# Kernel optimization log

Hardware: AMD Instinct MI355X
Metric: run time of the kernel (lower is better)

Reference implementation:

```python
import jax, jax.numpy as jnp
import numpy as np

MAX_WORDS = 256  # = batch['labels'].shape[1]


def _align(hidden, word_ids, max_words):
    """Batched segment-mean: (B,S,D) subtoken states -> (B,max_words,D) word states.
    Equivalent to align_subtokens_to_words applied per sample (word_ids all valid)."""
    B, S, D = hidden.shape
    seg = (word_ids.astype(jnp.int32) + jnp.arange(B, dtype=jnp.int32)[:, None] * max_words).reshape(-1)
    sums = jax.ops.segment_sum(hidden.reshape(-1, D), seg, num_segments=B * max_words)
    cnts = jax.ops.segment_sum(jnp.ones((B * S,), hidden.dtype), seg, num_segments=B * max_words)
    out = jnp.where(cnts[:, None] > 0, sums / jnp.maximum(cnts, 1.0)[:, None], 0.0)
    return out.reshape(B, max_words, D)


def setup_inputs() -> dict:
    key = jax.random.key(0)
    ks = jax.random.split(key, 8)
    B, S, D, W = 64, 512, 768, MAX_WORDS
    h_hing_sub = jax.random.normal(ks[0], (B, S, D), dtype=jnp.float32)
    h_rob_sub = jax.random.normal(ks[1], (B, S, D), dtype=jnp.float32)
    hing_word_ids = jnp.sort(jax.random.randint(ks[2], (B, S), 0, W), axis=-1).astype(jnp.int32)
    rob_word_ids = jnp.sort(jax.random.randint(ks[3], (B, S), 0, W), axis=-1).astype(jnp.int32)
    num_words = jax.random.randint(ks[4], (B,), 1, W).astype(jnp.int32)
    router_w1 = jax.random.normal(ks[5], (2 * D, 256), dtype=jnp.float32) * (1.0 / np.sqrt(2 * D))
    router_b1 = jnp.zeros((256,), jnp.float32)
    router_w2 = jax.random.normal(ks[6], (256, 1), dtype=jnp.float32) * (1.0 / 16.0)
    router_b2 = jnp.zeros((1,), jnp.float32)
    head_w = jax.random.normal(ks[7], (D, 7), dtype=jnp.float32) * (1.0 / np.sqrt(D))
    head_b = jnp.zeros((7,), jnp.float32)
    return {
        'h_hing_sub': h_hing_sub, 'h_rob_sub': h_rob_sub,
        'hing_word_ids': hing_word_ids, 'rob_word_ids': rob_word_ids,
        'num_words': num_words,
        'router_w1': router_w1, 'router_b1': router_b1,
        'router_w2': router_w2, 'router_b2': router_b2,
        'head_w': head_w, 'head_b': head_b,
    }


def reference(h_hing_sub, h_rob_sub, hing_word_ids, rob_word_ids, num_words,
              router_w1, router_b1, router_w2, router_b2, head_w, head_b):
    W = MAX_WORDS
    # scatter-mean subtokens -> words (the dominant custom-kernel op)
    h_hing = _align(h_hing_sub, hing_word_ids, W)   # (B, W, 768)
    h_rob = _align(h_rob_sub, rob_word_ids, W)      # (B, W, 768)
    # token-level MLP router on concatenated word states (router_input='both')
    router_in = jnp.concatenate([h_hing, h_rob], axis=-1)             # (B, W, 1536)
    hdn = jax.nn.relu(jnp.einsum('bwd,dh->bwh', router_in, router_w1) + router_b1)
    alpha = jax.nn.sigmoid(jnp.einsum('bwh,ho->bwo', hdn, router_w2) + router_b2)  # (B, W, 1)
    blended = alpha * h_hing + (1.0 - alpha) * h_rob                  # (B, W, 768)
    logits = jnp.einsum('bwd,dl->bwl', blended, head_w) + head_b      # (B, W, num_labels)
    l2_disagreement = jnp.linalg.norm(h_hing - h_rob, axis=-1)        # (B, W)
    return logits, alpha.squeeze(-1), l2_disagreement
```

## Files before the change

kernel.cpp:

```cpp
#include <hip/hip_runtime.h>
#include <hip/hip_bf16.h>
#include <math.h>

#define BATCH 64
#define SEQ   512
#define DIM   768
#define NW    256
#define NT    (BATCH * NW)
#define KDIM  1536
#define HID   256
#define NL    7

#define BM  32
#define BK  64
#define BKP 72
#define NKT (KDIM / BK)

typedef __bf16 bf16_t;
typedef bf16_t bf16x4 __attribute__((ext_vector_type(4)));
typedef bf16_t bf16x8 __attribute__((ext_vector_type(8)));
typedef float  f32x4  __attribute__((ext_vector_type(4)));

__device__ __forceinline__ void madv(f32x4& a, const f32x4& v, float s) {
    a[0] = fmaf(v[0], s, a[0]);
    a[1] = fmaf(v[1], s, a[1]);
    a[2] = fmaf(v[2], s, a[2]);
    a[3] = fmaf(v[3], s, a[3]);
}

__global__ __launch_bounds__(256) void convert_w1_kernel(
    const float* __restrict__ w1, bf16_t* __restrict__ w1t)
{
    int kc = blockIdx.x >> 3;
    int kg = blockIdx.x & 7;
    int n  = threadIdx.x;
    bf16x8 v;
    #pragma unroll
    for (int j = 0; j < 8; j++)
        v[j] = (bf16_t)w1[(size_t)(kc * 64 + kg * 8 + j) * HID + n];
    *(bf16x8*)(w1t + (size_t)kc * (HID * BK) + n * BK + kg * 8) = v;
}

__global__ __launch_bounds__(256) void starts_kernel(
    const int* __restrict__ idh, const int* __restrict__ idr,
    int* __restrict__ starts)
{
    int blk = blockIdx.x;
    int t = blk >> 6;
    int b = blk & 63;
    const int* ids = (t ? idr : idh) + b * SEQ;
    int w = threadIdx.x;
    int lo = 0, hi = SEQ;
    while (lo < hi) {
        int m = (lo + hi) >> 1;
        if (ids[m] < w) lo = m + 1; else hi = m;
    }
    int* row = starts + blk * 257;
    row[w] = lo;
    if (w == 0) row[256] = SEQ;
}

__global__ __launch_bounds__(256, 2) void align_kernel(
    const float* __restrict__ hh, const float* __restrict__ hr,
    const int* __restrict__ starts, bf16_t* __restrict__ X)
{
    int tid  = threadIdx.x;
    int lane = tid & 63;
    int wv   = tid >> 6;
    int task = blockIdx.x * 4 + wv;
    int b = task >> 7;
    int t = (task >> 6) & 1;
    int c = task & 63;
    int w0 = c * 4;

    const int*   st    = starts + (t * 64 + b) * 257;
    const f32x4* base4 = (const f32x4*)((t ? hr : hh) + (size_t)b * SEQ * DIM);
    bf16_t*      dstb  = X + (size_t)b * NW * KDIM + t * DIM;

    int lo = st[w0];
    #pragma unroll 1
    for (int w = w0; w < w0 + 4; w++) {
        int hi = st[w + 1];
        int ns = __builtin_amdgcn_readfirstlane(hi - lo);
        bf16_t* xr = dstb + (size_t)w * KDIM;

        if (ns <= 0) {
            bf16x4 z = {};
            *(bf16x4*)(xr + lane * 4)         = z;
            *(bf16x4*)(xr + (lane + 64) * 4)  = z;
            *(bf16x4*)(xr + (lane + 128) * 4) = z;
        } else {
            int nm1 = ns - 1;
            const f32x4* p0 = base4 + (size_t)lo * 192;
            const f32x4* p1 = base4 + (size_t)(lo + (1 < ns ? 1 : nm1)) * 192;
            const f32x4* p2 = base4 + (size_t)(lo + (2 < ns ? 2 : nm1)) * 192;
            const f32x4* p3 = base4 + (size_t)(lo + (3 < ns ? 3 : nm1)) * 192;
            const f32x4* p4 = base4 + (size_t)(lo + (4 < ns ? 4 : nm1)) * 192;
            const f32x4* p5 = base4 + (size_t)(lo + (5 < ns ? 5 : nm1)) * 192;

            f32x4 l0a = p0[lane], l0b = p0[lane + 64], l0c = p0[lane + 128];
            f32x4 l1a = p1[lane], l1b = p1[lane + 64], l1c = p1[lane + 128];
            f32x4 l2a = p2[lane], l2b = p2[lane + 64], l2c = p2[lane + 128];
            f32x4 l3a = p3[lane], l3b = p3[lane + 64], l3c = p3[lane + 128];
            f32x4 l4a = p4[lane], l4b = p4[lane + 64], l4c = p4[lane + 128];
            f32x4 l5a = p5[lane], l5b = p5[lane + 64], l5c = p5[lane + 128];

            float k1 = (1 < ns) ? 1.f : 0.f;
            float k2 = (2 < ns) ? 1.f : 0.f;
            float k3 = (3 < ns) ? 1.f : 0.f;
            float k4 = (4 < ns) ? 1.f : 0.f;
            float k5 = (5 < ns) ? 1.f : 0.f;

            f32x4 a0 = l0a, a1 = l0b, a2 = l0c;
            madv(a0, l1a, k1); madv(a1, l1b, k1); madv(a2, l1c, k1);
            madv(a0, l2a, k2); madv(a1, l2b, k2); madv(a2, l2c, k2);
            madv(a0, l3a, k3); madv(a1, l3b, k3); madv(a2, l3c, k3);
            madv(a0, l4a, k4); madv(a1, l4b, k4); madv(a2, l4c, k4);
            madv(a0, l5a, k5); madv(a1, l5b, k5); madv(a2, l5c, k5);

            if (ns > 6) {
                for (int s = lo + 6; s < lo + ns; s++) {
                    const f32x4* r = base4 + (size_t)s * 192;
                    a0 += r[lane]; a1 += r[lane + 64]; a2 += r[lane + 128];
                }
            }

            float inv = 1.0f / (float)ns;
            bf16x4 o0, o1, o2;
            #pragma unroll
            for (int e = 0; e < 4; e++) {
                o0[e] = (bf16_t)(a0[e] * inv);
                o1[e] = (bf16_t)(a1[e] * inv);
                o2[e] = (bf16_t)(a2[e] * inv);
            }
            *(bf16x4*)(xr + lane * 4)         = o0;
            *(bf16x4*)(xr + (lane + 64) * 4)  = o1;
            *(bf16x4*)(xr + (lane + 128) * 4) = o2;
        }
        lo = hi;
    }
}

__global__ __launch_bounds__(256) void gemm_alpha_kernel(
    const bf16_t* __restrict__ X, const bf16_t* __restrict__ w1t,
    const float* __restrict__ b1, const float* __restrict__ w2,
    const float* __restrict__ b2, float* __restrict__ out)
{
    __shared__ __align__(16) bf16_t Xs[BM][BKP];
    __shared__ __align__(16) bf16_t Ws[HID][BKP];
    __shared__ float alpha_acc[BM];

    int tid   = threadIdx.x;
    int lane  = tid & 63;
    int wv    = tid >> 6;
    int row16 = lane & 15;
    int quad  = lane >> 4;
    int tok0  = blockIdx.x * BM;

    f32x4 acc[2][4];
    #pragma unroll
    for (int mi = 0; mi < 2; mi++)
        #pragma unroll
        for (int ni = 0; ni < 4; ni++)
            acc[mi][ni] = (f32x4){0.f, 0.f, 0.f, 0.f};

    int xr = tid >> 3;
    int xc = tid & 7;

    for (int kc = 0; kc < NKT; kc++) {
        {
            const uint4* src = (const uint4*)(X + (size_t)(tok0 + xr) * KDIM + kc * BK + xc * 8);
            *(uint4*)(&Xs[xr][xc * 8]) = *src;
        }
        {
            const uint4* srcb = (const uint4*)(w1t + (size_t)kc * (HID * BK));
            #pragma unroll
            for (int i = 0; i < 8; i++) {
                int cidx = tid + i * 256;
                *(uint4*)(&Ws[cidx >> 3][(cidx & 7) * 8]) = srcb[cidx];
            }
        }
        __syncthreads();
        #pragma unroll
        for (int kk2 = 0; kk2 < 2; kk2++) {
            bf16x8 af[2], bfg[4];
            #pragma unroll
            for (int mi = 0; mi < 2; mi++)
                af[mi] = *(const bf16x8*)(&Xs[mi * 16 + row16][kk2 * 32 + quad * 8]);
            #pragma unroll
            for (int ni = 0; ni < 4; ni++)
                bfg[ni] = *(const bf16x8*)(&Ws[wv * 64 + ni * 16 + row16][kk2 * 32 + quad * 8]);
            #pragma unroll
            for (int mi = 0; mi < 2; mi++)
                #pragma unroll
                for (int ni = 0; ni < 4; ni++)
                    acc[mi][ni] = __builtin_amdgcn_mfma_f32_16x16x32_bf16(
                        af[mi], bfg[ni], acc[mi][ni], 0, 0, 0);
        }
        __syncthreads();
    }

    float w2v[4], b1v[4];
    #pragma unroll
    for (int ni = 0; ni < 4; ni++) {
        int col = wv * 64 + ni * 16 + row16;
        w2v[ni] = w2[col];
        b1v[ni] = b1[col];
    }
    if (tid < BM) alpha_acc[tid] = 0.f;
    __syncthreads();

    #pragma unroll
    for (int mi = 0; mi < 2; mi++) {
        #pragma unroll
        for (int r = 0; r < 4; r++) {
            float p = 0.f;
            #pragma unroll
            for (int ni = 0; ni < 4; ni++) {
                float v = acc[mi][ni][r] + b1v[ni];
                v = v > 0.f ? v : 0.f;
                p += v * w2v[ni];
            }
            p += __shfl_xor(p, 1);
            p += __shfl_xor(p, 2);
            p += __shfl_xor(p, 4);
            p += __shfl_xor(p, 8);
            if (row16 == 0)
                atomicAdd(&alpha_acc[mi * 16 + quad * 4 + r], p);
        }
    }
    __syncthreads();
    if (tid < BM) {
        float a = 1.f / (1.f + expf(-(alpha_acc[tid] + b2[0])));
        out[(size_t)NT * NL + tok0 + tid] = a;
    }
}

__global__ __launch_bounds__(256) void blend_kernel(
    const bf16_t* __restrict__ X, const float* __restrict__ hw,
    const float* __restrict__ hb, float* __restrict__ out)
{
    __shared__ float hws[NL * DIM];
    int tid  = threadIdx.x;
    int lane = tid & 63;
    int wv   = tid >> 6;

    for (int i = tid; i < DIM * NL; i += 256) {
        int d = i / NL, l = i - d * NL;
        hws[l * DIM + d] = hw[i];
    }
    __syncthreads();

    int g   = lane >> 3;
    int u   = lane & 7;
    int tok = blockIdx.x * 32 + wv * 8 + g;

    float a = out[(size_t)NT * NL + tok];
    const bf16_t* xrow = X + (size_t)tok * KDIM;

    float lg[NL] = {0.f, 0.f, 0.f, 0.f, 0.f, 0.f, 0.f};
    float l2 = 0.f;

    #pragma unroll
    for (int k = 0; k < 12; k++) {
        int d0 = (k * 8 + u) * 8;
        bf16x8 hp = *(const bf16x8*)(xrow + d0);
        bf16x8 rp = *(const bf16x8*)(xrow + DIM + d0);
        float bl[8];
        #pragma unroll
        for (int e = 0; e < 8; e++) {
            float hhv = (float)hp[e];
            float hrv = (float)rp[e];
            float df  = hhv - hrv;
            bl[e] = fmaf(a, df, hrv);
            l2 = fmaf(df, df, l2);
        }
        #pragma unroll
        for (int l = 0; l < NL; l++) {
            f32x4 wA = *(const f32x4*)(&hws[l * DIM + d0]);
            f32x4 wB = *(const f32x4*)(&hws[l * DIM + d0 + 4]);
            lg[l] += bl[0]*wA[0] + bl[1]*wA[1] + bl[2]*wA[2] + bl[3]*wA[3]
                   + bl[4]*wB[0] + bl[5]*wB[1] + bl[6]*wB[2] + bl[7]*wB[3];
        }
    }

    #pragma unroll
    for (int off = 1; off < 8; off <<= 1) {
        #pragma unroll
        for (int l = 0; l < NL; l++) lg[l] += __shfl_xor(lg[l], off);
        l2 += __shfl_xor(l2, off);
    }

    if (u < NL) {
        float v = (u == 0) ? lg[0] : (u == 1) ? lg[1] : (u == 2) ? lg[2]
                : (u == 3) ? lg[3] : (u == 4) ? lg[4] : (u == 5) ? lg[5] : lg[6];
        out[(size_t)tok * NL + u] = v + hb[u];
    } else {
        out[(size_t)NT * NL + NT + tok] = sqrtf(l2);
    }
}

extern "C" void kernel_launch(void* const* d_in, const int* in_sizes, int n_in,
                              void* d_out, int out_size, void* d_ws, size_t ws_size,
                              hipStream_t stream)
{
    const float* hh  = (const float*)d_in[0];
    const float* hr  = (const float*)d_in[1];
    const int*   idh = (const int*)d_in[2];
    const int*   idr = (const int*)d_in[3];
    const float* w1  = (const float*)d_in[5];
    const float* b1  = (const float*)d_in[6];
    const float* w2  = (const float*)d_in[7];
    const float* b2  = (const float*)d_in[8];
    const float* hw  = (const float*)d_in[9];
    const float* hb  = (const float*)d_in[10];
    float* out = (float*)d_out;

    bf16_t* X      = (bf16_t*)d_ws;
    bf16_t* w1t    = X + (size_t)NT * KDIM;
    int*    starts = (int*)(w1t + (size_t)NKT * HID * BK);

    convert_w1_kernel<<<192, 256, 0, stream>>>(w1, w1t);
    starts_kernel<<<128, 256, 0, stream>>>(idh, idr, starts);
    align_kernel<<<2048, 256, 0, stream>>>(hh, hr, starts, X);
    gemm_alpha_kernel<<<NT / BM, 256, 0, stream>>>(X, w1t, b1, w2, b2, out);
    blend_kernel<<<512, 256, 0, stream>>>(X, hw, hb, out);
}
```

Baseline: 291.1 us.

## Fuse router GEMM with blend/head and restructure align as streaming segment scan

Folds the blend/logits/L2 stage into the router GEMM kernel, which now uses 512 threads and 64-token tiles. The blend step reads alpha from shared memory and reuses the W1 tile buffer to hold the head weights, so one launch and the alpha round-trip through global memory go away. The align kernel now has each wave stream a contiguous subtoken range covering 32 words over a 256-element slice of the hidden dimension. It reads word ids through readlane, flushes a mean whenever the word changes, and zero-fills empty words. This cuts per-word launch overhead and keeps loads sequential, at the cost of serialized boundary handling and fewer blocks.

```diff
diff --git a/kernel.cpp b/kernel.cpp
--- a/kernel.cpp
+++ b/kernel.cpp
@@ -11,7 +11,7 @@
 #define HID   256
 #define NL    7
 
-#define BM  32
+#define BM  64
 #define BK  64
 #define BKP 72
 #define NKT (KDIM / BK)
@@ -20,13 +20,6 @@
 typedef bf16_t bf16x4 __attribute__((ext_vector_type(4)));
 typedef bf16_t bf16x8 __attribute__((ext_vector_type(8)));
 typedef float  f32x4  __attribute__((ext_vector_type(4)));
-
-__device__ __forceinline__ void madv(f32x4& a, const f32x4& v, float s) {
-    a[0] = fmaf(v[0], s, a[0]);
-    a[1] = fmaf(v[1], s, a[1]);
-    a[2] = fmaf(v[2], s, a[2]);
-    a[3] = fmaf(v[3], s, a[3]);
-}
 
 __global__ __launch_bounds__(256) void convert_w1_kernel(
     const float* __restrict__ w1, bf16_t* __restrict__ w1t)
@@ -60,99 +53,100 @@
     if (w == 0) row[256] = SEQ;
 }
 
-__global__ __launch_bounds__(256, 2) void align_kernel(
+__global__ __launch_bounds__(256) void align_kernel(
     const float* __restrict__ hh, const float* __restrict__ hr,
+    const int* __restrict__ idh, const int* __restrict__ idr,
     const int* __restrict__ starts, bf16_t* __restrict__ X)
 {
     int tid  = threadIdx.x;
     int lane = tid & 63;
     int wv   = tid >> 6;
     int task = blockIdx.x * 4 + wv;
-    int b = task >> 7;
-    int t = (task >> 6) & 1;
-    int c = task & 63;
-    int w0 = c * 4;
-
-    const int*   st    = starts + (t * 64 + b) * 257;
-    const f32x4* base4 = (const f32x4*)((t ? hr : hh) + (size_t)b * SEQ * DIM);
-    bf16_t*      dstb  = X + (size_t)b * NW * KDIM + t * DIM;
-
-    int lo = st[w0];
-    #pragma unroll 1
-    for (int w = w0; w < w0 + 4; w++) {
-        int hi = st[w + 1];
-        int ns = __builtin_amdgcn_readfirstlane(hi - lo);
-        bf16_t* xr = dstb + (size_t)w * KDIM;
-
-        if (ns <= 0) {
+    int q  = task & 7;
+    int r3 = task >> 3;
+    int sl = r3 % 3;
+    int bt = r3 / 3;
+    int b  = bt >> 1;
+    int t  = bt & 1;
+    int w0 = q * 32;
+
+    const int*   st   = starts + (t * 64 + b) * 257;
+    const int*   ids  = (t ? idr : idh) + b * SEQ;
+    const f32x4* base = (const f32x4*)((t ? hr : hh) + (size_t)b * SEQ * DIM) + sl * 64;
+    bf16_t*      dst  = X + (size_t)b * NW * KDIM + t * DIM + sl * 256 + lane * 4;
+
+    int sLo = st[w0];
+    int sHi = st[w0 + 32];
+
+    f32x4 acc = {0.f, 0.f, 0.f, 0.f};
+    int   cnt = 0;
+    int   w   = w0;
+
+    for (int sb = sLo; sb < sHi; sb += 8) {
+        int smax = sHi - 1;
+        f32x4 v0 = base[(size_t)(sb     < smax ? sb     : smax) * 192 + lane];
+        f32x4 v1 = base[(size_t)(sb + 1 < smax ? sb + 1 : smax) * 192 + lane];
+        f32x4 v2 = base[(size_t)(sb + 2 < smax ? sb + 2 : smax) * 192 + lane];
+        f32x4 v3 = base[(size_t)(sb + 3 < smax ? sb + 3 : smax) * 192 + lane];
+        f32x4 v4 = base[(size_t)(sb + 4 < smax ? sb + 4 : smax) * 192 + lane];
+        f32x4 v5 = base[(size_t)(sb + 5 < smax ? sb + 5 : smax) * 192 + lane];
+        f32x4 v6 = base[(size_t)(sb + 6 < smax ? sb + 6 : smax) * 192 + lane];
+        f32x4 v7 = base[(size_t)(sb + 7 < smax ? sb + 7 : smax) * 192 + lane];
+        int myid = ids[(lane & 7) + sb < sHi ? (lane & 7) + sb : smax];
+
+        f32x4 vv[8] = {v0, v1, v2, v3, v4, v5, v6, v7};
+        #pragma unroll
+        for (int j = 0; j < 8; j++) {
+            int s = sb + j;
+            if (s >= sHi) break;
+            int wid = __builtin_amdgcn_readlane(myid, j);
+            if (wid != w) {
+                float inv = cnt > 0 ? 1.f / (float)cnt : 0.f;
+                bf16x4 o;
+                #pragma unroll
+                for (int e = 0; e < 4; e++) o[e] = (bf16_t)(acc[e] * inv);
+                *(bf16x4*)(dst + (size_t)w * KDIM) = o;
+                for (int ww = w + 1; ww < wid; ww++) {
+                    bf16x4 z = {};
+                    *(bf16x4*)(dst + (size_t)ww * KDIM) = z;
+                }
+                w = wid;
+                acc = (f32x4){0.f, 0.f, 0.f, 0.f};
+                cnt = 0;
+            }
+            acc += vv[j];
+            cnt++;
+        }
+    }
+    {
+        float inv = cnt > 0 ? 1.f / (float)cnt : 0.f;
+        bf16x4 o;
+        #pragma unroll
+        for (int e = 0; e < 4; e++) o[e] = (bf16_t)(acc[e] * inv);
+        *(bf16x4*)(dst + (size_t)w * KDIM) = o;
+        for (int ww = w + 1; ww < w0 + 32; ww++) {
             bf16x4 z = {};
-            *(bf16x4*)(xr + lane * 4)         = z;
-            *(bf16x4*)(xr + (lane + 64) * 4)  = z;
-            *(bf16x4*)(xr + (lane + 128) * 4) = z;
-        } else {
-            int nm1 = ns - 1;
-            const f32x4* p0 = base4 + (size_t)lo * 192;
-            const f32x4* p1 = base4 + (size_t)(lo + (1 < ns ? 1 : nm1)) * 192;
-            const f32x4* p2 = base4 + (size_t)(lo + (2 < ns ? 2 : nm1)) * 192;
-            const f32x4* p3 = base4 + (size_t)(lo + (3 < ns ? 3 : nm1)) * 192;
-            const f32x4* p4 = base4 + (size_t)(lo + (4 < ns ? 4 : nm1)) * 192;
-            const f32x4* p5 = base4 + (size_t)(lo + (5 < ns ? 5 : nm1)) * 192;
-
-            f32x4 l0a = p0[lane], l0b = p0[lane + 64], l0c = p0[lane + 128];
-            f32x4 l1a = p1[lane], l1b = p1[lane + 64], l1c = p1[lane + 128];
-            f32x4 l2a = p2[lane], l2b = p2[lane + 64], l2c = p2[lane + 128];
-            f32x4 l3a = p3[lane], l3b = p3[lane + 64], l3c = p3[lane + 128];
-            f32x4 l4a = p4[lane], l4b = p4[lane + 64], l4c = p4[lane + 128];
-            f32x4 l5a = p5[lane], l5b = p5[lane + 64], l5c = p5[lane + 128];
-
-            float k1 = (1 < ns) ? 1.f : 0.f;
-            float k2 = (2 < ns) ? 1.f : 0.f;
-            float k3 = (3 < ns) ? 1.f : 0.f;
-            float k4 = (4 < ns) ? 1.f : 0.f;
-            float k5 = (5 < ns) ? 1.f : 0.f;
-
-            f32x4 a0 = l0a, a1 = l0b, a2 = l0c;
-            madv(a0, l1a, k1); madv(a1, l1b, k1); madv(a2, l1c, k1);
-            madv(a0, l2a, k2); madv(a1, l2b, k2); madv(a2, l2c, k2);
-            madv(a0, l3a, k3); madv(a1, l3b, k3); madv(a2, l3c, k3);
-            madv(a0, l4a, k4); madv(a1, l4b, k4); madv(a2, l4c, k4);
-            madv(a0, l5a, k5); madv(a1, l5b, k5); madv(a2, l5c, k5);
-
-            if (ns > 6) {
-                for (int s = lo + 6; s < lo + ns; s++) {
-                    const f32x4* r = base4 + (size_t)s * 192;
-                    a0 += r[lane]; a1 += r[lane + 64]; a2 += r[lane + 128];
-                }
-            }
-
-            float inv = 1.0f / (float)ns;
-            bf16x4 o0, o1, o2;
-            #pragma unroll
-            for (int e = 0; e < 4; e++) {
-                o0[e] = (bf16_t)(a0[e] * inv);
-                o1[e] = (bf16_t)(a1[e] * inv);
-                o2[e] = (bf16_t)(a2[e] * inv);
-            }
-            *(bf16x4*)(xr + lane * 4)         = o0;
-            *(bf16x4*)(xr + (lane + 64) * 4)  = o1;
-            *(bf16x4*)(xr + (lane + 128) * 4) = o2;
-        }
-        lo = hi;
-    }
-}
-
-__global__ __launch_bounds__(256) void gemm_alpha_kernel(
+            *(bf16x4*)(dst + (size_t)ww * KDIM) = z;
+        }
+    }
+}
+
+__global__ __launch_bounds__(512) void fused_kernel(
     const bf16_t* __restrict__ X, const bf16_t* __restrict__ w1t,
     const float* __restrict__ b1, const float* __restrict__ w2,
-    const float* __restrict__ b2, float* __restrict__ out)
+    const float* __restrict__ b2, const float* __restrict__ hw,
+    const float* __restrict__ hb, float* __restrict__ out)
 {
     __shared__ __align__(16) bf16_t Xs[BM][BKP];
     __shared__ __align__(16) bf16_t Ws[HID][BKP];
     __shared__ float alpha_acc[BM];
+    __shared__ float alpha_s[BM];
 
     int tid   = threadIdx.x;
     int lane  = tid & 63;
     int wv    = tid >> 6;
+    int tg    = wv >> 2;
+    int cg    = wv & 3;
     int row16 = lane & 15;
     int quad  = lane >> 4;
     int tok0  = blockIdx.x * BM;
@@ -175,8 +169,8 @@
         {
             const uint4* srcb = (const uint4*)(w1t + (size_t)kc * (HID * BK));
             #pragma unroll
-            for (int i = 0; i < 8; i++) {
-                int cidx = tid + i * 256;
+            for (int i = 0; i < 4; i++) {
+                int cidx = tid + i * 512;
                 *(uint4*)(&Ws[cidx >> 3][(cidx & 7) * 8]) = srcb[cidx];
             }
         }
@@ -186,10 +180,10 @@
             bf16x8 af[2], bfg[4];
             #pragma unroll
             for (int mi = 0; mi < 2; mi++)
-                af[mi] = *(const bf16x8*)(&Xs[mi * 16 + row16][kk2 * 32 + quad * 8]);
+                af[mi] = *(const bf16x8*)(&Xs[tg * 32 + mi * 16 + row16][kk2 * 32 + quad * 8]);
             #pragma unroll
             for (int ni = 0; ni < 4; ni++)
-                bfg[ni] = *(const bf16x8*)(&Ws[wv * 64 + ni * 16 + row16][kk2 * 32 + quad * 8]);
+                bfg[ni] = *(const bf16x8*)(&Ws[cg * 64 + ni * 16 + row16][kk2 * 32 + quad * 8]);
             #pragma unroll
             for (int mi = 0; mi < 2; mi++)
                 #pragma unroll
@@ -203,7 +197,7 @@
     float w2v[4], b1v[4];
     #pragma unroll
     for (int ni = 0; ni < 4; ni++) {
-        int col = wv * 64 + ni * 16 + row16;
+        int col = cg * 64 + ni * 16 + row16;
         w2v[ni] = w2[col];
         b1v[ni] = b1[col];
     }
@@ -226,26 +220,19 @@
             p += __shfl_xor(p, 4);
             p += __shfl_xor(p, 8);
             if (row16 == 0)
-                atomicAdd(&alpha_acc[mi * 16 + quad * 4 + r], p);
+                atomicAdd(&alpha_acc[tg * 32 + mi * 16 + quad * 4 + r], p);
         }
     }
     __syncthreads();
     if (tid < BM) {
         float a = 1.f / (1.f + expf(-(alpha_acc[tid] + b2[0])));
+        alpha_s[tid] = a;
         out[(size_t)NT * NL + tok0 + tid] = a;
     }
-}
-
-__global__ __launch_bounds__(256) void blend_kernel(
-    const bf16_t* __restrict__ X, const float* __restrict__ hw,
-    const float* __restrict__ hb, float* __restrict__ out)
-{
-    __shared__ float hws[NL * DIM];
-    int tid  = threadIdx.x;
-    int lane = tid & 63;
-    int wv   = tid >> 6;
-
-    for (int i = tid; i < DIM * NL; i += 256) {
+
+    float* hws = (float*)&Ws[0][0];
+    __syncthreads();
+    for (int i = tid; i < DIM * NL; i += 512) {
         int d = i / NL, l = i - d * NL;
         hws[l * DIM + d] = hw[i];
     }
@@ -253,9 +240,9 @@
 
     int g   = lane >> 3;
     int u   = lane & 7;
-    int tok = blockIdx.x * 32 + wv * 8 + g;
-
-    float a = out[(size_t)NT * NL + tok];
+    int tok = tok0 + wv * 8 + g;
+
+    float a = alpha_s[wv * 8 + g];
     const bf16_t* xrow = X + (size_t)tok * KDIM;
 
     float lg[NL] = {0.f, 0.f, 0.f, 0.f, 0.f, 0.f, 0.f};
@@ -322,7 +309,6 @@
 
     convert_w1_kernel<<<192, 256, 0, stream>>>(w1, w1t);
     starts_kernel<<<128, 256, 0, stream>>>(idh, idr, starts);
-    align_kernel<<<2048, 256, 0, stream>>>(hh, hr, starts, X);
-    gemm_alpha_kernel<<<NT / BM, 256, 0, stream>>>(X, w1t, b1, w2, b2, out);
-    blend_kernel<<<512, 256, 0, stream>>>(X, hw, hb, out);
-}
+    align_kernel<<<768, 256, 0, stream>>>(hh, hr, idh, idr, starts, X);
+    fused_kernel<<<NT / BM, 512, 0, stream>>>(X, w1t, b1, w2, b2, hw, hb, out);
+}
```

Measured after the change: 292.8 us. Within noise of the previous version (+0.6%).
